# Kernel tuning notes

Hardware: AMD Instinct MI355X
Metric: run time of the kernel (lower is better)

The kernel has to match this reference:

```python
import jax, jax.numpy as jnp
import numpy as np

D_MODEL = 256; D_STATE = 128; EXPAND = 2; HEADDIM = 64
D_INNER = EXPAND * D_MODEL            # 512
NHEADS = D_INNER // HEADDIM           # 8
CONV_DIM = D_INNER + 2 * D_STATE      # 768
D_IN_PROJ = 2 * D_INNER + 2 * D_STATE + NHEADS  # 1288
KCONV = 4
BATCH = 16; SEQ = 1024; CHUNK = 64
EPS = 1e-5


def setup_inputs() -> dict:
    key = jax.random.key(0)
    ks = jax.random.split(key, 8)
    # dt_bias = inverse-softplus of dt ~ U[1e-3, 1e-1] (Mamba2 init)
    dt = jnp.exp(jax.random.uniform(ks[3], (NHEADS,), jnp.float32,
                                    np.log(1e-3), np.log(1e-1)))
    dt_bias = dt + jnp.log(-jnp.expm1(-dt))
    return {
        "u": jax.random.normal(ks[0], (BATCH, SEQ, D_MODEL), jnp.float32),
        "W_in": 0.02 * jax.random.normal(ks[1], (D_MODEL, D_IN_PROJ), jnp.float32),
        "conv_w": 0.2 * jax.random.normal(ks[2], (CONV_DIM, KCONV), jnp.float32),
        "conv_b": jnp.zeros((CONV_DIM,), jnp.float32),
        "dt_bias": dt_bias,
        "A_log": jnp.log(jax.random.uniform(ks[4], (NHEADS,), jnp.float32, 1.0, 16.0)),
        "D": jnp.ones((NHEADS,), jnp.float32),
        "norm_w": jnp.ones((D_INNER,), jnp.float32),
        "W_out": 0.02 * jax.random.normal(ks[5], (D_INNER, D_MODEL), jnp.float32),
    }


def _segsum(x):
    # x: (..., L) -> (..., L, L) lower-triangular cumulative segment sums
    L = x.shape[-1]
    c = jnp.cumsum(x, axis=-1)
    ss = c[..., :, None] - c[..., None, :]
    mask = jnp.tril(jnp.ones((L, L), bool))
    return jnp.where(mask, ss, -jnp.inf)


def _ssd(X, A, Bm, Cm, chunk):
    # Chunked SSD selective scan (Mamba2, ngroups=1).
    # X:(b,t,h,p)  A:(b,t,h)  Bm,Cm:(b,t,n)
    b, t, h, p = X.shape
    nc = t // chunk
    X = X.reshape(b, nc, chunk, h, p)
    A = A.reshape(b, nc, chunk, h).transpose(0, 3, 1, 2)   # (b,h,c,l)
    Bm = Bm.reshape(b, nc, chunk, -1)
    Cm = Cm.reshape(b, nc, chunk, -1)
    A_cs = jnp.cumsum(A, axis=-1)                          # (b,h,c,l)
    Lmat = jnp.exp(_segsum(A))                             # (b,h,c,l,l)
    # within-chunk (diagonal) contribution
    Y_diag = jnp.einsum('bcln,bcsn,bhcls,bcshp->bclhp', Cm, Bm, Lmat, X)
    # per-chunk end states
    decay_states = jnp.exp(A_cs[..., -1:] - A_cs)          # (b,h,c,l)
    states = jnp.einsum('bcln,bhcl,bclhp->bchpn', Bm, decay_states, X)
    # inter-chunk recurrence (vectorized over chunks)
    A_chunk = jnp.pad(A_cs[..., -1], ((0, 0), (0, 0), (1, 0)))
    decay_chunk = jnp.exp(_segsum(A_chunk))                # (b,h,c+1,c+1)
    states = jnp.concatenate([jnp.zeros_like(states[:, :1]), states], axis=1)
    new_states = jnp.einsum('bhzc,bchpn->bzhpn', decay_chunk, states)
    states = new_states[:, :-1]                            # state entering each chunk
    Y_off = jnp.einsum('bcln,bchpn,bhcl->bclhp', Cm, states, jnp.exp(A_cs))
    return (Y_diag + Y_off).reshape(b, t, h, p)


def reference(u, W_in, conv_w, conv_b, dt_bias, A_log, D, norm_w, W_out):
    B, T, _ = u.shape
    zxbcdt = u @ W_in                                      # (B,T,1288)
    z, xBC, dt = jnp.split(zxbcdt, [D_INNER, D_INNER + CONV_DIM], axis=-1)
    # causal depthwise conv1d, kernel KCONV
    xp = jnp.pad(xBC, ((0, 0), (KCONV - 1, 0), (0, 0)))
    kern = conv_w.T[:, None, :]                            # (K,1,C)
    xBC = jax.lax.conv_general_dilated(
        xp, kern, (1,), 'VALID',
        dimension_numbers=('NWC', 'WIO', 'NWC'), feature_group_count=CONV_DIM)
    xBC = jax.nn.silu(xBC + conv_b)
    x, Bc, Cc = jnp.split(xBC, [D_INNER, D_INNER + D_STATE], axis=-1)
    x = x.reshape(B, T, NHEADS, HEADDIM)
    dt = jax.nn.softplus(dt + dt_bias)                     # (B,T,H)
    A = -jnp.exp(A_log)                                    # (H,)
    y = _ssd(x * dt[..., None], dt * A, Bc, Cc, CHUNK)     # (B,T,H,P)
    y = y + D[:, None] * x                                 # skip term
    y = y.reshape(B, T, D_INNER)
    # gated RMSNorm: norm(y * silu(z)) * weight
    g = y * jax.nn.silu(z)
    g = g * jax.lax.rsqrt(jnp.mean(g * g, axis=-1, keepdims=True) + EPS) * norm_w
    return g @ W_out
```

## Files before the change

kernel.cpp:

```cpp
#include <hip/hip_runtime.h>
#include <hip/hip_bf16.h>
#include <math.h>

#define BATCHN  16
#define SEQ     1024
#define DMODEL  256
#define DSTATE  128
#define HEADDIM 64
#define DINNER  512
#define NHEADS  8
#define CONVDIM 768
#define DINPROJ 1288
#define ZXLD    1280
#define KCONV   4
#define NCHUNK  16
#define LCHUNK  64
#define EPSV    1e-5f
#define ROWS    (BATCHN*SEQ)

typedef __attribute__((ext_vector_type(8))) __bf16 bf16x8;
typedef __attribute__((ext_vector_type(4))) float  f32x4;

__device__ inline ushort f2bf(float f) {
    union { float f; uint32_t u; } v; v.f = f;
    uint32_t r = v.u + 0x7fff + ((v.u >> 16) & 1);
    return (ushort)(r >> 16);
}
__device__ inline float bf2f(ushort u) {
    union { uint32_t u; float f; } v; v.u = ((uint32_t)u) << 16;
    return v.f;
}

__global__ __launch_bounds__(256) void prep_k(const float* __restrict__ u,
                                              const float* __restrict__ W_in,
                                              const float* __restrict__ W_out,
                                              const float* __restrict__ dt_bias,
                                              const float* __restrict__ A_log,
                                              ushort* __restrict__ ubf,
                                              float* __restrict__ dtb,
                                              float* __restrict__ adtb,
                                              ushort* __restrict__ WtA,
                                              ushort* __restrict__ WtB) {
    __shared__ union {
        struct { float Uld[32][264]; float Ws[DMODEL][NHEADS]; } d;
        float Ts[32][33];
    } S;
    const int tid = threadIdx.x;
    if (blockIdx.x < 512) {
        #pragma unroll
        for (int j = 0; j < 8; ++j) {
            int idx = tid + j * 256;
            S.d.Ws[idx >> 3][idx & 7] = W_in[(size_t)(idx >> 3) * DINPROJ + 1280 + (idx & 7)];
        }
        const int row0 = blockIdx.x * 32;
        #pragma unroll
        for (int v = 0; v < 8; ++v) {
            int e = v * 1024 + tid * 4;
            int r = e >> 8, cc = e & 255;
            float4 x = *(const float4*)&u[(size_t)(row0 + r) * DMODEL + cc];
            *(float4*)&S.d.Uld[r][cc] = x;
            ushort t4[4];
            t4[0]=f2bf(x.x); t4[1]=f2bf(x.y); t4[2]=f2bf(x.z); t4[3]=f2bf(x.w);
            *(ushort4*)&ubf[(size_t)(row0 + r) * DMODEL + cc] = *(ushort4*)t4;
        }
        __syncthreads();
        const int row = tid >> 3, h = tid & 7;
        float acc = 0.f;
        #pragma unroll 8
        for (int k = 0; k < DMODEL; k += 4) {
            float4 uv = *(const float4*)&S.d.Uld[row][k];
            acc += uv.x * S.d.Ws[k][h] + uv.y * S.d.Ws[k+1][h]
                 + uv.z * S.d.Ws[k+2][h] + uv.w * S.d.Ws[k+3][h];
        }
        float v = acc + dt_bias[h];
        float dt = (v > 20.f) ? v : log1pf(__expf(v));
        dtb [(size_t)(row0 + row) * NHEADS + h] = dt;
        adtb[(size_t)(row0 + row) * NHEADS + h] = dt * (-__expf(A_log[h]));
    } else {
        int bid = blockIdx.x - 512;
        const float* src; ushort* dst; int K, ldsrc, nx;
        if (bid < 320) { src = W_in;  dst = WtA; K = DMODEL; ldsrc = DINPROJ; nx = 40; }
        else { bid -= 320; src = W_out; dst = WtB; K = DINNER; ldsrc = DMODEL; nx = 8; }
        const int n0 = (bid % nx) * 32, k0 = (bid / nx) * 32;
        const int tx = tid & 31, ty = tid >> 5;
        #pragma unroll
        for (int j = 0; j < 4; ++j) {
            int kl = ty * 4 + j;
            S.Ts[kl][tx] = src[(size_t)(k0 + kl) * ldsrc + n0 + tx];
        }
        __syncthreads();
        #pragma unroll
        for (int j = 0; j < 4; ++j) {
            int nl = ty * 4 + j;
            dst[(size_t)(n0 + nl) * K + k0 + tx] = f2bf(S.Ts[tx][nl]);
        }
    }
}

#define LDSW 72
template<typename CT>
__global__ __launch_bounds__(256) void gemm_bf16(const ushort* __restrict__ A,
                                                 const ushort* __restrict__ Bt,
                                                 CT* __restrict__ C,
                                                 int M, int N, int K, int nx) {
    __shared__ ushort As[128 * LDSW];
    __shared__ ushort Bs[128 * LDSW];
    const int tid  = threadIdx.x;
    const int nwg  = gridDim.x;
    const int work = (blockIdx.x & 7) * (nwg >> 3) + (blockIdx.x >> 3);
    const int m0 = (work / nx) * 128, n0 = (work % nx) * 128;
    const int wid = tid >> 6, lane = tid & 63;
    const int wr = wid >> 1, wc = wid & 1;
    const int r = tid >> 1, kq = tid & 1;
    const int fr = lane & 15, kc = lane >> 4;

    f32x4 acc[4][4];
    #pragma unroll
    for (int i = 0; i < 4; ++i)
        #pragma unroll
        for (int j = 0; j < 4; ++j) acc[i][j] = (f32x4)0.f;

    for (int kt = 0; kt < K; kt += 64) {
        const ushort* ap = &A [(size_t)(m0 + r) * K + kt + kq * 32];
        const ushort* bp = &Bt[(size_t)(n0 + r) * K + kt + kq * 32];
        #pragma unroll
        for (int v = 0; v < 4; ++v) {
            *(uint4*)&As[r * LDSW + kq * 32 + v * 8] = *(const uint4*)(ap + v * 8);
            *(uint4*)&Bs[r * LDSW + kq * 32 + v * 8] = *(const uint4*)(bp + v * 8);
        }
        __syncthreads();
        #pragma unroll
        for (int kk = 0; kk < 2; ++kk) {
            bf16x8 af[4], bfv[4];
            #pragma unroll
            for (int i = 0; i < 4; ++i) {
                af[i]  = *(const bf16x8*)&As[(wr * 64 + i * 16 + fr) * LDSW + kk * 32 + kc * 8];
                bfv[i] = *(const bf16x8*)&Bs[(wc * 64 + i * 16 + fr) * LDSW + kk * 32 + kc * 8];
            }
            #pragma unroll
            for (int i = 0; i < 4; ++i)
                #pragma unroll
                for (int j = 0; j < 4; ++j)
                    acc[i][j] = __builtin_amdgcn_mfma_f32_16x16x32_bf16(af[i], bfv[j], acc[i][j], 0, 0, 0);
        }
        __syncthreads();
    }
    #pragma unroll
    for (int i = 0; i < 4; ++i)
        #pragma unroll
        for (int j = 0; j < 4; ++j)
            #pragma unroll
            for (int q = 0; q < 4; ++q) {
                int rr = m0 + wr * 64 + i * 16 + (lane >> 4) * 4 + q;
                int cc = n0 + wc * 64 + j * 16 + (lane & 15);
                if constexpr (sizeof(CT) == 4) C[(size_t)rr * N + cc] = acc[i][j][q];
                else                           C[(size_t)rr * N + cc] = f2bf(acc[i][j][q]);
            }
}

__global__ __launch_bounds__(256) void conv_silu_k(const ushort* __restrict__ zx,
                                                   const float* __restrict__ cw,
                                                   const float* __restrict__ cb,
                                                   ushort* __restrict__ out) {
    __shared__ float cws[KCONV][CONVDIM];
    __shared__ float cbs[CONVDIM];
    const int tid = threadIdx.x;
    #pragma unroll
    for (int it = 0; it < 3; ++it) {
        int i = tid + it * 256;
        cbs[i] = cb[i];
        #pragma unroll
        for (int k = 0; k < KCONV; ++k) cws[k][i] = cw[i * KCONV + k];
    }
    __syncthreads();

    const int idx = blockIdx.x * 256 + tid;
    const int cg = idx % 96, btq = idx / 96;
    const int c0 = cg * 8;
    const int bt0 = btq * 4;
    const int t0 = bt0 & (SEQ - 1);

    float wv[KCONV][8], bias[8];
    #pragma unroll
    for (int j = 0; j < 8; ++j) bias[j] = cbs[c0 + j];
    #pragma unroll
    for (int k = 0; k < KCONV; ++k) {
        float4 a = *(const float4*)&cws[k][c0];
        float4 b = *(const float4*)&cws[k][c0 + 4];
        wv[k][0] = a.x; wv[k][1] = a.y; wv[k][2] = a.z; wv[k][3] = a.w;
        wv[k][4] = b.x; wv[k][5] = b.y; wv[k][6] = b.z; wv[k][7] = b.w;
    }
    float xr[7][8];
    #pragma unroll
    for (int r = 0; r < 7; ++r) {
        int tt = t0 - 3 + r;
        if (tt >= 0) {
            uint4 v = *(const uint4*)&zx[(size_t)(bt0 - 3 + r) * ZXLD + DINNER + c0];
            const ushort* pv = (const ushort*)&v;
            #pragma unroll
            for (int j = 0; j < 8; ++j) xr[r][j] = bf2f(pv[j]);
        } else {
            #pragma unroll
            for (int j = 0; j < 8; ++j) xr[r][j] = 0.f;
        }
    }
    #pragma unroll
    for (int dt = 0; dt < 4; ++dt) {
        float acc[8];
        #pragma unroll
        for (int j = 0; j < 8; ++j) acc[j] = bias[j];
        #pragma unroll
        for (int k = 0; k < KCONV; ++k)
            #pragma unroll
            for (int j = 0; j < 8; ++j) acc[j] += xr[dt + k][j] * wv[k][j];
        ushort res[8];
        #pragma unroll
        for (int j = 0; j < 8; ++j)
            res[j] = f2bf(acc[j] / (1.f + __expf(-acc[j])));
        *(uint4*)&out[(size_t)(bt0 + dt) * CONVDIM + c0] = *(uint4*)res;
    }
}

#define SLDA 136
#define SLDB 72
__global__ __launch_bounds__(256) void ssd_mfma_k(const ushort* __restrict__ xbc,
                                                  const float* __restrict__ dtb,
                                                  const float* __restrict__ adtb,
                                                  const float* __restrict__ Dp,
                                                  ushort* __restrict__ ybuf,
                                                  ushort* __restrict__ states,
                                                  float* __restrict__ acsbuf,
                                                  float* __restrict__ chunksum) {
    const int wk = (blockIdx.x & 7) * 64 + (blockIdx.x >> 3);
    const int hgrp = wk & 1, c = (wk >> 1) & 15, b = wk >> 5;
    const int row0 = b * SEQ + c * LCHUNK;
    const int tid = threadIdx.x;
    const int lane = tid & 63, w = tid >> 6;
    const int fr = lane & 15, kc = lane >> 4;

    __shared__ union {
        struct { ushort Bs[64][SLDA]; ushort Cs[64][SLDA]; } p1;
        struct { ushort Ps[64][SLDB]; ushort Xt[64][SLDB]; ushort Xdt[64][SLDB]; } p2;
    } U;
    __shared__ ushort Btr[128][SLDB];
    __shared__ float acs4[4][64];
    __shared__ float dts[4][64];
    __shared__ float decs[4][64];

    {
        const int hh = hgrp * 4 + w;
        float v = adtb[(size_t)(row0 + lane) * NHEADS + hh];
        #pragma unroll
        for (int off = 1; off < 64; off <<= 1) {
            float t = __shfl_up(v, off);
            if (lane >= off) v += t;
        }
        acs4[w][lane] = v;
        float tot = __shfl(v, 63);
        decs[w][lane] = __expf(tot - v);
        acsbuf[(((size_t)b * NCHUNK + c) * NHEADS + hh) * LCHUNK + lane] = v;
        if (lane == 63) chunksum[((size_t)b * NCHUNK + c) * NHEADS + hh] = v;
        dts[w][lane] = dtb[(size_t)(row0 + lane) * NHEADS + hh];
    }
    for (int it = 0; it < 4; ++it) {
        int idx = tid + it * 256;
        int l = idx >> 4, ng = idx & 15;
        const ushort* rp = &xbc[(size_t)(row0 + l) * CONVDIM + DINNER];
        uint4 vb = *(const uint4*)(rp + ng * 8);
        *(uint4*)&U.p1.Bs[l][ng * 8] = vb;
        uint4 vc = *(const uint4*)(rp + DSTATE + ng * 8);
        *(uint4*)&U.p1.Cs[l][ng * 8] = vc;
        const ushort* pv = (const ushort*)&vb;
        #pragma unroll
        for (int j = 0; j < 8; ++j) Btr[ng * 8 + j][l] = pv[j];
    }
    __syncthreads();

    const int wr = w >> 1, wc = w & 1;
    f32x4 accG[2][2];
    #pragma unroll
    for (int i = 0; i < 2; ++i)
        #pragma unroll
        for (int j = 0; j < 2; ++j) accG[i][j] = (f32x4)0.f;
    #pragma unroll
    for (int kt = 0; kt < 4; ++kt) {
        bf16x8 af[2], bfv[2];
        #pragma unroll
        for (int i = 0; i < 2; ++i) af[i]  = *(const bf16x8*)&U.p1.Cs[wr*32 + i*16 + fr][kt*32 + kc*8];
        #pragma unroll
        for (int j = 0; j < 2; ++j) bfv[j] = *(const bf16x8*)&U.p1.Bs[wc*32 + j*16 + fr][kt*32 + kc*8];
        #pragma unroll
        for (int i = 0; i < 2; ++i)
            #pragma unroll
            for (int j = 0; j < 2; ++j)
                accG[i][j] = __builtin_amdgcn_mfma_f32_16x16x32_bf16(af[i], bfv[j], accG[i][j], 0, 0, 0);
    }
    __syncthreads();

    for (int hl = 0; hl < 4; ++hl) {
        const int hh = hgrp * 4 + hl;
        {
            const int p = lane;
            ushort xt[16], xdt[16];
            #pragma unroll
            for (int j = 0; j < 16; ++j) {
                int l = w * 16 + j;
                float xv = bf2f(xbc[(size_t)(row0 + l) * CONVDIM + hh * HEADDIM + p])
                           * dts[hl][l];
                xt[j]  = f2bf(xv);
                xdt[j] = f2bf(xv * decs[hl][l]);
            }
            #pragma unroll
            for (int v = 0; v < 4; ++v) {
                *(ushort4*)&U.p2.Xt [p][w*16 + v*4] = *(ushort4*)&xt[v*4];
                *(ushort4*)&U.p2.Xdt[p][w*16 + v*4] = *(ushort4*)&xdt[v*4];
            }
        }
        #pragma unroll
        for (int i = 0; i < 2; ++i)
            #pragma unroll
            for (int j = 0; j < 2; ++j)
                #pragma unroll
                for (int q = 0; q < 4; ++q) {
                    int l = wr*32 + i*16 + (lane >> 4)*4 + q;
                    int s = wc*32 + j*16 + fr;
                    float v = 0.f;
                    if (s < l)       v = accG[i][j][q] * __expf(acs4[hl][l] - acs4[hl][s]);
                    else if (s == l) v = accG[i][j][q] + Dp[hh] / dts[hl][l];
                    U.p2.Ps[l][s] = f2bf(v);
                }
        __syncthreads();
        {
            f32x4 acc[4];
            #pragma unroll
            for (int j = 0; j < 4; ++j) acc[j] = (f32x4)0.f;
            #pragma unroll
            for (int kt = 0; kt < 2; ++kt) {
                bf16x8 af = *(const bf16x8*)&U.p2.Ps[w*16 + fr][kt*32 + kc*8];
                #pragma unroll
                for (int j = 0; j < 4; ++j) {
                    bf16x8 bfv = *(const bf16x8*)&U.p2.Xt[j*16 + fr][kt*32 + kc*8];
                    acc[j] = __builtin_amdgcn_mfma_f32_16x16x32_bf16(af, bfv, acc[j], 0, 0, 0);
                }
            }
            #pragma unroll
            for (int j = 0; j < 4; ++j)
                #pragma unroll
                for (int q = 0; q < 4; ++q) {
                    int l = w*16 + (lane >> 4)*4 + q;
                    int p = j*16 + fr;
                    ybuf[(size_t)(row0 + l) * DINNER + hh * HEADDIM + p] = f2bf(acc[j][q]);
                }
        }
        {
            f32x4 acc2[4][2];
            #pragma unroll
            for (int mt = 0; mt < 4; ++mt)
                #pragma unroll
                for (int jt = 0; jt < 2; ++jt) acc2[mt][jt] = (f32x4)0.f;
            #pragma unroll
            for (int kt = 0; kt < 2; ++kt) {
                bf16x8 a4[4], b2[2];
                #pragma unroll
                for (int mt = 0; mt < 4; ++mt) a4[mt] = *(const bf16x8*)&U.p2.Xdt[mt*16 + fr][kt*32 + kc*8];
                #pragma unroll
                for (int jt = 0; jt < 2; ++jt) b2[jt] = *(const bf16x8*)&Btr[w*32 + jt*16 + fr][kt*32 + kc*8];
                #pragma unroll
                for (int mt = 0; mt < 4; ++mt)
                    #pragma unroll
                    for (int jt = 0; jt < 2; ++jt)
                        acc2[mt][jt] = __builtin_amdgcn_mfma_f32_16x16x32_bf16(a4[mt], b2[jt], acc2[mt][jt], 0, 0, 0);
            }
            ushort* sb = states + ((((size_t)b * NCHUNK + c) * NHEADS + hh) * HEADDIM) * DSTATE;
            #pragma unroll
            for (int mt = 0; mt < 4; ++mt)
                #pragma unroll
                for (int jt = 0; jt < 2; ++jt)
                    #pragma unroll
                    for (int q = 0; q < 4; ++q) {
                        int p = mt*16 + (lane >> 4)*4 + q;
                        int n = w*32 + jt*16 + fr;
                        sb[(size_t)p * DSTATE + n] = f2bf(acc2[mt][jt][q]);
                    }
        }
        __syncthreads();
    }
}

__global__ __launch_bounds__(256) void scan_k(ushort* __restrict__ states,
                                              const float* __restrict__ chunksum) {
    const int bid = blockIdx.x;
    const int pq = bid & 3, h = (bid >> 2) & 7, b = bid >> 5;
    const int tid = threadIdx.x;
    float pref[8];
    #pragma unroll
    for (int k = 0; k < 8; ++k) pref[k] = 0.f;
    for (int c = 0; c < NCHUNK; ++c) {
        ushort* base = states + (((size_t)b * NCHUNK + c) * NHEADS + h) * (HEADDIM * DSTATE)
                       + pq * 2048 + tid * 8;
        float dec = __expf(chunksum[((size_t)b * NCHUNK + c) * NHEADS + h]);
        uint4 v = *(const uint4*)base;
        const ushort* pv = (const ushort*)&v;
        ushort outv[8];
        #pragma unroll
        for (int j = 0; j < 8; ++j) {
            float cur = bf2f(pv[j]);
            outv[j] = f2bf(pref[j]);
            pref[j] = dec * pref[j] + cur;
        }
        *(uint4*)base = *(uint4*)outv;
    }
}

#define YLDS 520
__global__ __launch_bounds__(256) void yoff_gate_k(const ushort* __restrict__ xbc,
                                                   const ushort* __restrict__ states,
                                                   const float* __restrict__ acsbuf,
                                                   const ushort* __restrict__ ybuf,
                                                   const ushort* __restrict__ zx,
                                                   const float* __restrict__ nw,
                                                   ushort* __restrict__ gbuf) {
    const int c = blockIdx.x, b = blockIdx.y;
    const int row0 = b * SEQ + c * LCHUNK;
    const int tid = threadIdx.x;
    const int lane = tid & 63, w = tid >> 6;
    const int fr = lane & 15, kc = lane >> 4;
    __shared__ ushort Csh[64][SLDA];
    __shared__ ushort Ssh[64][SLDA];
    __shared__ ushort Ys[64][YLDS];
    __shared__ float eah[64];

    for (int it = 0; it < 4; ++it) {
        int idx = tid + it * 256;
        int l = idx >> 4, ng = idx & 15;
        *(uint4*)&Csh[l][ng * 8] =
            *(const uint4*)&xbc[(size_t)(row0 + l) * CONVDIM + DINNER + DSTATE + ng * 8];
    }
    for (int hl = 0; hl < NHEADS; ++hl) {
        __syncthreads();
        const ushort* sb = states + ((((size_t)b * NCHUNK + c) * NHEADS + hl) * HEADDIM) * DSTATE;
        for (int it = 0; it < 4; ++it) {
            int idx = tid + it * 256;
            int p = idx >> 4, ng = idx & 15;
            *(uint4*)&Ssh[p][ng * 8] = *(const uint4*)&sb[(size_t)p * DSTATE + ng * 8];
        }
        if (tid < 64)
            eah[tid] = __expf(acsbuf[(((size_t)b * NCHUNK + c) * NHEADS + hl) * LCHUNK + tid]);
        __syncthreads();
        f32x4 acc[4];
        #pragma unroll
        for (int j = 0; j < 4; ++j) acc[j] = (f32x4)0.f;
        #pragma unroll
        for (int kt = 0; kt < 4; ++kt) {
            bf16x8 af = *(const bf16x8*)&Csh[w*16 + fr][kt*32 + kc*8];
            #pragma unroll
            for (int j = 0; j < 4; ++j) {
                bf16x8 bfv = *(const bf16x8*)&Ssh[j*16 + fr][kt*32 + kc*8];
                acc[j] = __builtin_amdgcn_mfma_f32_16x16x32_bf16(af, bfv, acc[j], 0, 0, 0);
            }
        }
        #pragma unroll
        for (int j = 0; j < 4; ++j)
            #pragma unroll
            for (int q = 0; q < 4; ++q) {
                int l = w*16 + (lane >> 4)*4 + q;
                int p = j*16 + fr;
                float val = bf2f(ybuf[(size_t)(row0 + l) * DINNER + hl * HEADDIM + p])
                            + acc[j][q] * eah[l];
                Ys[l][hl * HEADDIM + p] = f2bf(val);
            }
    }
    __syncthreads();
    float nwv[8];
    #pragma unroll
    for (int j = 0; j < 8; ++j) nwv[j] = nw[lane * 8 + j];
    for (int i = 0; i < 16; ++i) {
        int l = w * 16 + i;
        int row = row0 + l;
        uint4 zv = *(const uint4*)&zx[(size_t)row * ZXLD + lane * 8];
        const ushort* pz = (const ushort*)&zv;
        float g[8], ss = 0.f;
        #pragma unroll
        for (int j = 0; j < 8; ++j) {
            float y = bf2f(Ys[l][lane * 8 + j]);
            float z = bf2f(pz[j]);
            float sz = z / (1.f + __expf(-z));
            g[j] = y * sz;
            ss += g[j] * g[j];
        }
        #pragma unroll
        for (int off = 32; off; off >>= 1) ss += __shfl_xor(ss, off);
        float r = rsqrtf(ss / (float)DINNER + EPSV);
        ushort res[8];
        #pragma unroll
        for (int j = 0; j < 8; ++j) res[j] = f2bf(g[j] * r * nwv[j]);
        *(uint4*)&gbuf[(size_t)row * DINNER + lane * 8] = *(uint4*)res;
    }
}

extern "C" void kernel_launch(void* const* d_in, const int* in_sizes, int n_in,
                              void* d_out, int out_size, void* d_ws, size_t ws_size,
                              hipStream_t stream) {
    const float* u       = (const float*)d_in[0];
    const float* W_in    = (const float*)d_in[1];
    const float* conv_w  = (const float*)d_in[2];
    const float* conv_b  = (const float*)d_in[3];
    const float* dt_bias = (const float*)d_in[4];
    const float* A_log   = (const float*)d_in[5];
    const float* Dp      = (const float*)d_in[6];
    const float* norm_w  = (const float*)d_in[7];
    const float* W_out   = (const float*)d_in[8];
    float* out = (float*)d_out;

    char* p = (char*)d_ws;
    ushort* zx       = (ushort*)p; p += (size_t)ROWS * ZXLD * sizeof(ushort);
    ushort* ybuf     = (ushort*)p; p += (size_t)ROWS * DINNER * sizeof(ushort);
    ushort* gbuf     = (ushort*)p; p += (size_t)ROWS * DINNER * sizeof(ushort);
    ushort* states   = (ushort*)p; p += (size_t)BATCHN * NCHUNK * NHEADS * HEADDIM * DSTATE * sizeof(ushort);
    ushort* xbc      = (ushort*)p; p += (size_t)ROWS * CONVDIM * sizeof(ushort);
    ushort* ubf      = (ushort*)p; p += (size_t)ROWS * DMODEL * sizeof(ushort);
    float*  dtb      = (float*)p;  p += (size_t)ROWS * NHEADS  * sizeof(float);
    float*  adtb     = (float*)p;  p += (size_t)ROWS * NHEADS  * sizeof(float);
    float*  chunksum = (float*)p;  p += (size_t)BATCHN * NCHUNK * NHEADS * sizeof(float);
    float*  acsbuf   = (float*)p;  p += (size_t)BATCHN * NCHUNK * NHEADS * LCHUNK * sizeof(float);
    ushort* WtA      = (ushort*)p; p += (size_t)ZXLD * DMODEL * sizeof(ushort);
    ushort* WtB      = (ushort*)p; p += (size_t)DMODEL * DINNER * sizeof(ushort);

    prep_k<<<960, 256, 0, stream>>>(u, W_in, W_out, dt_bias, A_log,
                                    ubf, dtb, adtb, WtA, WtB);
    gemm_bf16<ushort><<<(ZXLD/128)*(ROWS/128), 256, 0, stream>>>(
        ubf, WtA, zx, ROWS, ZXLD, DMODEL, ZXLD/128);
    conv_silu_k<<<(ROWS/4)*96/256, 256, 0, stream>>>(zx, conv_w, conv_b, xbc);
    ssd_mfma_k<<<512, 256, 0, stream>>>(
        xbc, dtb, adtb, Dp, ybuf, states, acsbuf, chunksum);
    scan_k<<<BATCHN*NHEADS*4, 256, 0, stream>>>(states, chunksum);
    yoff_gate_k<<<dim3(NCHUNK, BATCHN), 256, 0, stream>>>(
        xbc, states, acsbuf, ybuf, zx, norm_w, gbuf);
    gemm_bf16<float><<<(DMODEL/128)*(ROWS/128), 256, 0, stream>>>(
        gbuf, WtB, out, ROWS, DMODEL, DINNER, DMODEL/128);
}
```

Baseline: 130.2 us.

## Stage bf16 GEMM output through LDS and split yoff_gate into half-chunk blocks

The bf16 GEMM epilogue now writes the accumulator tile into reused LDS and then stores it to global memory as coalesced 16-byte rows, replacing scattered 2-byte stores. The yoff_gate kernel now processes 32-row half chunks across 512 blocks instead of 256 full-chunk blocks, with an XCD-aware block remapping. Each wave computes two output tiles instead of four. This is meant to improve occupancy and store efficiency, at the cost of loading each state tile twice and adding an extra barrier in the GEMM epilogue.

```diff
diff --git a/kernel.cpp b/kernel.cpp
--- a/kernel.cpp
+++ b/kernel.cpp
@@ -98,13 +98,15 @@
 }
 
 #define LDSW 72
+#define TILEC 132
 template<typename CT>
 __global__ __launch_bounds__(256) void gemm_bf16(const ushort* __restrict__ A,
                                                  const ushort* __restrict__ Bt,
                                                  CT* __restrict__ C,
                                                  int M, int N, int K, int nx) {
-    __shared__ ushort As[128 * LDSW];
-    __shared__ ushort Bs[128 * LDSW];
+    __shared__ ushort LB[2 * 128 * LDSW];
+    ushort* As = LB;
+    ushort* Bs = LB + 128 * LDSW;
     const int tid  = threadIdx.x;
     const int nwg  = gridDim.x;
     const int work = (blockIdx.x & 7) * (nwg >> 3) + (blockIdx.x >> 3);
@@ -145,17 +147,35 @@
         }
         __syncthreads();
     }
-    #pragma unroll
-    for (int i = 0; i < 4; ++i)
-        #pragma unroll
-        for (int j = 0; j < 4; ++j)
-            #pragma unroll
-            for (int q = 0; q < 4; ++q) {
-                int rr = m0 + wr * 64 + i * 16 + (lane >> 4) * 4 + q;
-                int cc = n0 + wc * 64 + j * 16 + (lane & 15);
-                if constexpr (sizeof(CT) == 4) C[(size_t)rr * N + cc] = acc[i][j][q];
-                else                           C[(size_t)rr * N + cc] = f2bf(acc[i][j][q]);
-            }
+    if constexpr (sizeof(CT) == 4) {
+        #pragma unroll
+        for (int i = 0; i < 4; ++i)
+            #pragma unroll
+            for (int j = 0; j < 4; ++j)
+                #pragma unroll
+                for (int q = 0; q < 4; ++q) {
+                    int rr = m0 + wr * 64 + i * 16 + (lane >> 4) * 4 + q;
+                    int cc = n0 + wc * 64 + j * 16 + (lane & 15);
+                    C[(size_t)rr * N + cc] = acc[i][j][q];
+                }
+    } else {
+        ushort (*Tile)[TILEC] = (ushort (*)[TILEC])LB;
+        #pragma unroll
+        for (int i = 0; i < 4; ++i)
+            #pragma unroll
+            for (int j = 0; j < 4; ++j)
+                #pragma unroll
+                for (int q = 0; q < 4; ++q)
+                    Tile[wr * 64 + i * 16 + (lane >> 4) * 4 + q]
+                        [wc * 64 + j * 16 + (lane & 15)] = f2bf(acc[i][j][q]);
+        __syncthreads();
+        #pragma unroll
+        for (int it = 0; it < 8; ++it) {
+            int idx = tid + it * 256;
+            int rr = idx >> 4, g = idx & 15;
+            *(uint4*)&C[(size_t)(m0 + rr) * N + n0 + g * 8] = *(uint4*)&Tile[rr][g * 8];
+        }
+    }
 }
 
 __global__ __launch_bounds__(256) void conv_silu_k(const ushort* __restrict__ zx,
@@ -412,7 +432,6 @@
     }
 }
 
-#define YLDS 520
 __global__ __launch_bounds__(256) void yoff_gate_k(const ushort* __restrict__ xbc,
                                                    const ushort* __restrict__ states,
                                                    const float* __restrict__ acsbuf,
@@ -420,17 +439,21 @@
                                                    const ushort* __restrict__ zx,
                                                    const float* __restrict__ nw,
                                                    ushort* __restrict__ gbuf) {
-    const int c = blockIdx.x, b = blockIdx.y;
-    const int row0 = b * SEQ + c * LCHUNK;
+    const int wk = (blockIdx.x & 7) * 64 + (blockIdx.x >> 3);
+    const int half = wk & 1, c = (wk >> 1) & 15, b = wk >> 5;
+    const int row0 = b * SEQ + c * LCHUNK + half * 32;
     const int tid = threadIdx.x;
     const int lane = tid & 63, w = tid >> 6;
     const int fr = lane & 15, kc = lane >> 4;
-    __shared__ ushort Csh[64][SLDA];
+    const int rw = (w & 1) * 16;
+    const int j0 = (w >> 1) * 2;
+    __shared__ ushort Csh[32][SLDA];
     __shared__ ushort Ssh[64][SLDA];
-    __shared__ ushort Ys[64][YLDS];
-    __shared__ float eah[64];
-
-    for (int it = 0; it < 4; ++it) {
+    __shared__ ushort Ys[32][520];
+    __shared__ float eah[32];
+
+    #pragma unroll
+    for (int it = 0; it < 2; ++it) {
         int idx = tid + it * 256;
         int l = idx >> 4, ng = idx & 15;
         *(uint4*)&Csh[l][ng * 8] =
@@ -439,34 +462,35 @@
     for (int hl = 0; hl < NHEADS; ++hl) {
         __syncthreads();
         const ushort* sb = states + ((((size_t)b * NCHUNK + c) * NHEADS + hl) * HEADDIM) * DSTATE;
+        #pragma unroll
         for (int it = 0; it < 4; ++it) {
             int idx = tid + it * 256;
             int p = idx >> 4, ng = idx & 15;
             *(uint4*)&Ssh[p][ng * 8] = *(const uint4*)&sb[(size_t)p * DSTATE + ng * 8];
         }
-        if (tid < 64)
-            eah[tid] = __expf(acsbuf[(((size_t)b * NCHUNK + c) * NHEADS + hl) * LCHUNK + tid]);
-        __syncthreads();
-        f32x4 acc[4];
-        #pragma unroll
-        for (int j = 0; j < 4; ++j) acc[j] = (f32x4)0.f;
+        if (tid < 32)
+            eah[tid] = __expf(acsbuf[(((size_t)b * NCHUNK + c) * NHEADS + hl) * LCHUNK
+                                     + half * 32 + tid]);
+        __syncthreads();
+        f32x4 acc[2];
+        acc[0] = (f32x4)0.f; acc[1] = (f32x4)0.f;
         #pragma unroll
         for (int kt = 0; kt < 4; ++kt) {
-            bf16x8 af = *(const bf16x8*)&Csh[w*16 + fr][kt*32 + kc*8];
-            #pragma unroll
-            for (int j = 0; j < 4; ++j) {
-                bf16x8 bfv = *(const bf16x8*)&Ssh[j*16 + fr][kt*32 + kc*8];
-                acc[j] = __builtin_amdgcn_mfma_f32_16x16x32_bf16(af, bfv, acc[j], 0, 0, 0);
-            }
-        }
-        #pragma unroll
-        for (int j = 0; j < 4; ++j)
+            bf16x8 af = *(const bf16x8*)&Csh[rw + fr][kt*32 + kc*8];
+            #pragma unroll
+            for (int jj = 0; jj < 2; ++jj) {
+                bf16x8 bfv = *(const bf16x8*)&Ssh[(j0+jj)*16 + fr][kt*32 + kc*8];
+                acc[jj] = __builtin_amdgcn_mfma_f32_16x16x32_bf16(af, bfv, acc[jj], 0, 0, 0);
+            }
+        }
+        #pragma unroll
+        for (int jj = 0; jj < 2; ++jj)
             #pragma unroll
             for (int q = 0; q < 4; ++q) {
-                int l = w*16 + (lane >> 4)*4 + q;
-                int p = j*16 + fr;
+                int l = rw + (lane >> 4)*4 + q;
+                int p = (j0+jj)*16 + fr;
                 float val = bf2f(ybuf[(size_t)(row0 + l) * DINNER + hl * HEADDIM + p])
-                            + acc[j][q] * eah[l];
+                            + acc[jj][q] * eah[l];
                 Ys[l][hl * HEADDIM + p] = f2bf(val);
             }
     }
@@ -474,8 +498,9 @@
     float nwv[8];
     #pragma unroll
     for (int j = 0; j < 8; ++j) nwv[j] = nw[lane * 8 + j];
-    for (int i = 0; i < 16; ++i) {
-        int l = w * 16 + i;
+    #pragma unroll
+    for (int i = 0; i < 8; ++i) {
+        int l = w * 8 + i;
         int row = row0 + l;
         uint4 zv = *(const uint4*)&zx[(size_t)row * ZXLD + lane * 8];
         const ushort* pz = (const ushort*)&zv;
@@ -534,7 +559,7 @@
     ssd_mfma_k<<<512, 256, 0, stream>>>(
         xbc, dtb, adtb, Dp, ybuf, states, acsbuf, chunksum);
     scan_k<<<BATCHN*NHEADS*4, 256, 0, stream>>>(states, chunksum);
-    yoff_gate_k<<<dim3(NCHUNK, BATCHN), 256, 0, stream>>>(
+    yoff_gate_k<<<512, 256, 0, stream>>>(
         xbc, states, acsbuf, ybuf, zx, norm_w, gbuf);
     gemm_bf16<float><<<(DMODEL/128)*(ROWS/128), 256, 0, stream>>>(
         gbuf, WtB, out, ROWS, DMODEL, DINNER, DMODEL/128);
```

Result: faster. 125.4 us, median of 2 (-3.7%).
